# Kernel tuning notes

Measured on AMD Instinct MI355X. Metric: run time of the kernel, lower is better.

Reference implementation:

```python
import jax, jax.numpy as jnp
import numpy as np

N_NODES = 50000
N_EDGES = 1600000
IN_DIM, HID, HEADS, OUT_DIM = 128, 32, 4, 16
NEG_SLOPE = 0.2  # DGL GATConv default


def setup_inputs() -> dict:
    key = jax.random.key(0)
    ks = jax.random.split(key, 12)
    features = jax.random.normal(ks[0], (N_NODES, IN_DIM), dtype=jnp.float32)
    src = jax.random.randint(ks[1], (N_EDGES,), 0, N_NODES, dtype=jnp.int32)
    dst = jax.random.randint(ks[2], (N_EDGES,), 0, N_NODES, dtype=jnp.int32)
    # layer 1 params (xavier-style scale)
    W1 = jax.random.normal(ks[3], (IN_DIM, HEADS * HID), dtype=jnp.float32) * (2.0 / (IN_DIM + HEADS * HID)) ** 0.5
    al1 = jax.random.normal(ks[4], (HEADS, HID), dtype=jnp.float32) * 0.1
    ar1 = jax.random.normal(ks[5], (HEADS, HID), dtype=jnp.float32) * 0.1
    b1 = jnp.zeros((HEADS * HID,), dtype=jnp.float32)
    # layer 2 params
    W2 = jax.random.normal(ks[6], (HID, OUT_DIM), dtype=jnp.float32) * (2.0 / (HID + OUT_DIM)) ** 0.5
    al2 = jax.random.normal(ks[7], (1, OUT_DIM), dtype=jnp.float32) * 0.1
    ar2 = jax.random.normal(ks[8], (1, OUT_DIM), dtype=jnp.float32) * 0.1
    b2 = jnp.zeros((OUT_DIM,), dtype=jnp.float32)
    return {"features": features, "src": src, "dst": dst,
            "W1": W1, "al1": al1, "ar1": ar1, "b1": b1,
            "W2": W2, "al2": al2, "ar2": ar2, "b2": b2}


def gat_conv(x, src, dst, W, al, ar, b, n_nodes):
    """DGL GATConv (no dropout, no residual). Returns [N, H, out]."""
    H, out = al.shape
    feat = (x @ W).reshape(-1, H, out)                       # [N,H,out]
    el = jnp.sum(feat * al, axis=-1)                         # [N,H]
    er = jnp.sum(feat * ar, axis=-1)                         # [N,H]
    e = jax.nn.leaky_relu(el[src] + er[dst], NEG_SLOPE)      # [E,H]
    # segment softmax over incoming edges per destination node
    m = jax.ops.segment_max(e, dst, num_segments=n_nodes)    # [N,H]
    ex = jnp.exp(e - m[dst])                                 # [E,H]
    s = jax.ops.segment_sum(ex, dst, num_segments=n_nodes)   # [N,H]
    alpha = ex / s[dst]                                      # [E,H]
    msg = alpha[:, :, None] * feat[src]                      # [E,H,out]
    rst = jax.ops.segment_sum(msg, dst, num_segments=n_nodes)
    return rst + b.reshape(H, out)


def reference(features, src, dst, W1, al1, ar1, b1, W2, al2, ar2, b2):
    n = features.shape[0]
    x1 = gat_conv(features, src, dst, W1, al1, ar1, b1, n)   # [N,HEADS,HID]
    x1 = jnp.mean(jax.nn.relu(x1), axis=1)                   # [N,HID]
    x2 = gat_conv(x1, src, dst, W2, al2, ar2, b2, n)         # [N,1,OUT]
    x2 = jnp.squeeze(x2, axis=1)                             # [N,OUT]
    return jax.nn.log_softmax(x2, axis=-1)
```

## Files before the change

### kernel.cpp

```cpp
#include <hip/hip_runtime.h>
#include <math.h>

#define NEG_SLOPE 0.2f
#define BINCAP 10240

typedef __attribute__((ext_vector_type(8))) short short8;
typedef __attribute__((ext_vector_type(4))) float f32x4;
typedef __attribute__((ext_vector_type(2))) float f32x2;

__device__ __forceinline__ float lrelu(float x) {
    return x >= 0.f ? x : NEG_SLOPE * x;
}
__device__ __forceinline__ unsigned bf16_rne(float f) {
    unsigned b = __float_as_uint(f);
    return (b + 0x7FFFu + ((b >> 16) & 1u)) >> 16;
}

__global__ __launch_bounds__(256) void prep(
    const float* __restrict__ W, unsigned short* __restrict__ Wt,
    int* __restrict__ bin_cursor)
{
    if (blockIdx.x == 64) {
        bin_cursor[threadIdx.x] = threadIdx.x * BINCAP;
        return;
    }
    int i = blockIdx.x * 256 + threadIdx.x;
    int kin = i >> 7, nout = i & 127;
    Wt[nout * 128 + kin] = (unsigned short)bf16_rne(W[kin * 128 + nout]);
}

__global__ __launch_bounds__(256) void scatter_bins(
    const int* __restrict__ src, const int* __restrict__ dst,
    int* __restrict__ bin_cursor, unsigned* __restrict__ binned,
    int E, int nbins)
{
    __shared__ unsigned stage[3328];
    __shared__ int hist[256];
    __shared__ int base_l[256];
    int tid = threadIdx.x;
    hist[tid] = 0;
    __syncthreads();
    int epb = (E + gridDim.x - 1) / gridDim.x;
    int beg = blockIdx.x * epb, end = min(E, beg + epb);
    int cnt_local = end - beg;
    for (int k = tid; k < cnt_local; k += 256) {
        int d = dst[beg + k];
        stage[k] = ((unsigned)d << 16) | (unsigned)src[beg + k];
        atomicAdd(&hist[d >> 8], 1);
    }
    __syncthreads();
    if (tid < nbins) {
        int c = hist[tid];
        base_l[tid] = (c > 0) ? atomicAdd(&bin_cursor[tid], c) : 0;
    }
    __syncthreads();
    hist[tid] = 0;
    __syncthreads();
    for (int k = tid; k < cnt_local; k += 256) {
        unsigned w = stage[k];
        int bin = w >> 24;
        int slot = atomicAdd(&hist[bin], 1);
        binned[base_l[bin] + slot] = w;
    }
}

__global__ __launch_bounds__(256) void local_sort(
    const unsigned* __restrict__ binned, const int* __restrict__ bin_cursor,
    int* __restrict__ rowptr, unsigned short* __restrict__ deg,
    unsigned short* __restrict__ csr, int N, int nbins)
{
    __shared__ int cnt[256];
    __shared__ int sh[256];
    int b = blockIdx.x;
    int t = threadIdx.x;
    int gbase = b * BINCAP;
    int gcount = bin_cursor[b] - gbase;
    cnt[t] = 0;
    __syncthreads();
    for (int i = t; i < gcount; i += 256)
        atomicAdd(&cnt[(binned[gbase + i] >> 16) & 255], 1);
    __syncthreads();
    int own = cnt[t];
    sh[t] = own;
    __syncthreads();
#pragma unroll
    for (int off = 1; off < 256; off <<= 1) {
        int v = (t >= off) ? sh[t - off] : 0;
        __syncthreads();
        sh[t] += v;
        __syncthreads();
    }
    int excl = sh[t] - own;
    int dcount = min(256, N - (b << 8));
    if (t < dcount) {
        rowptr[(b << 8) + t] = gbase + excl;
        deg[(b << 8) + t] = (unsigned short)own;
    }
    cnt[t] = excl;
    __syncthreads();
    for (int i = t; i < gcount; i += 256) {
        unsigned w = binned[gbase + i];
        int slot = atomicAdd(&cnt[(w >> 16) & 255], 1);
        csr[gbase + slot] = (unsigned short)(w & 0xFFFFu);
    }
}

__global__ __launch_bounds__(256) void gemm1_mfma(
    const float* __restrict__ X, const unsigned short* __restrict__ Wt,
    const float* __restrict__ al, const float* __restrict__ ar,
    unsigned short* __restrict__ feat1b, float* __restrict__ el1,
    float* __restrict__ er1, int N)
{
    __shared__ unsigned short Xb[64][136];
    __shared__ unsigned short Wb[128][136];
    int tid = threadIdx.x;
    int nb = blockIdx.x * 64;

    for (int idx = tid; idx < 128 * 16; idx += 256) {
        int row = idx >> 4, q = idx & 15;
        *(uint4*)&Wb[row][q * 8] = *(const uint4*)&Wt[row * 128 + q * 8];
    }
    for (int idx = tid; idx < 64 * 32; idx += 256) {
        int row = idx >> 5, q = idx & 31;
        int n = nb + row;
        float4 v = (n < N) ? *(const float4*)&X[(size_t)n * 128 + q * 4]
                           : make_float4(0.f, 0.f, 0.f, 0.f);
        unsigned lo = bf16_rne(v.x) | (bf16_rne(v.y) << 16);
        unsigned hi = bf16_rne(v.z) | (bf16_rne(v.w) << 16);
        *(uint2*)&Xb[row][q * 4] = make_uint2(lo, hi);
    }
    __syncthreads();

    int wave = tid >> 6, lane = tid & 63;
    int m = lane & 15, quad = lane >> 4;
    f32x4 acc[8];
#pragma unroll
    for (int t = 0; t < 8; ++t) acc[t] = (f32x4){0.f, 0.f, 0.f, 0.f};

#pragma unroll
    for (int kt = 0; kt < 4; ++kt) {
        int k0 = kt * 32 + quad * 8;
        short8 a = *(const short8*)&Xb[wave * 16 + m][k0];
#pragma unroll
        for (int t = 0; t < 8; ++t) {
            short8 b = *(const short8*)&Wb[t * 16 + m][k0];
            acc[t] = __builtin_amdgcn_mfma_f32_16x16x32_bf16(a, b, acc[t], 0, 0, 0);
        }
    }

    float al_lo[4], al_hi[4], ar_lo[4], ar_hi[4];
#pragma unroll
    for (int h = 0; h < 4; ++h) {
        al_lo[h] = al[h * 32 + m];       al_hi[h] = al[h * 32 + 16 + m];
        ar_lo[h] = ar[h * 32 + m];       ar_hi[h] = ar[h * 32 + 16 + m];
    }

#pragma unroll
    for (int r = 0; r < 4; ++r) {
        int n = nb + wave * 16 + quad * 4 + r;
        float pel[4], per[4];
#pragma unroll
        for (int h = 0; h < 4; ++h) {
            float fa = acc[2 * h][r], fb = acc[2 * h + 1][r];
            pel[h] = fa * al_lo[h] + fb * al_hi[h];
            per[h] = fa * ar_lo[h] + fb * ar_hi[h];
        }
#pragma unroll
        for (int off = 1; off < 16; off <<= 1) {
#pragma unroll
            for (int h = 0; h < 4; ++h) {
                pel[h] += __shfl_xor(pel[h], off);
                per[h] += __shfl_xor(per[h], off);
            }
        }
        if (n < N) {
#pragma unroll
            for (int t = 0; t < 8; ++t)
                feat1b[(size_t)n * 128 + t * 16 + m] =
                    (unsigned short)bf16_rne(acc[t][r]);
            if (m == 0) {
#pragma unroll
                for (int h = 0; h < 4; ++h) {
                    el1[(size_t)n * 4 + h] = pel[h];
                    er1[(size_t)n * 4 + h] = per[h];
                }
            }
        }
    }
}

__global__ __launch_bounds__(256) void agg1_fused(
    const int* __restrict__ rowptr, const unsigned short* __restrict__ deg,
    const unsigned short* __restrict__ csr,
    const unsigned short* __restrict__ feat1b, const float* __restrict__ el1,
    const float* __restrict__ er1, const float* __restrict__ b1,
    const float* __restrict__ W2, const float* __restrict__ al2,
    const float* __restrict__ ar2, unsigned short* __restrict__ feat2b,
    float* __restrict__ el2, float* __restrict__ er2, int N)
{
    __shared__ uint2 pairs[4][4][66];
    int gid = blockIdx.x * 256 + threadIdx.x;
    int d = gid >> 6;
    if (d >= N) return;
    int wv = (threadIdx.x >> 6) & 3;
    int lane = threadIdx.x & 63;
    int h = lane >> 4;
    float4 er4 = ((const float4*)er1)[d];
    int beg = rowptr[d], end = beg + (int)deg[d];
    const unsigned* feat32 = (const unsigned*)feat1b;

    float M = -INFINITY, S = 0.f;
    f32x2 A = {0.f, 0.f};

    for (int base = beg; base < end; base += 64) {
        int cnt = min(64, end - base);
        int sn = 0;
        float4 v = make_float4(-INFINITY, -INFINITY, -INFINITY, -INFINITY);
        if (lane < cnt) {
            sn = (int)csr[base + lane];
            float4 el4 = ((const float4*)el1)[sn];
            v.x = lrelu(el4.x + er4.x);
            v.y = lrelu(el4.y + er4.y);
            v.z = lrelu(el4.z + er4.z);
            v.w = lrelu(el4.w + er4.w);
        }
        float4 cm = v;
#pragma unroll
        for (int off = 1; off < 64; off <<= 1) {
            cm.x = fmaxf(cm.x, __shfl_xor(cm.x, off));
            cm.y = fmaxf(cm.y, __shfl_xor(cm.y, off));
            cm.z = fmaxf(cm.z, __shfl_xor(cm.z, off));
            cm.w = fmaxf(cm.w, __shfl_xor(cm.w, off));
        }
        float4 w;
        w.x = __expf(v.x - cm.x);
        w.y = __expf(v.y - cm.y);
        w.z = __expf(v.z - cm.z);
        w.w = __expf(v.w - cm.w);
        unsigned snb = (unsigned)sn << 6;
        pairs[wv][0][lane] = make_uint2(snb, __float_as_uint(w.x));
        pairs[wv][1][lane] = make_uint2(snb, __float_as_uint(w.y));
        pairs[wv][2][lane] = make_uint2(snb, __float_as_uint(w.z));
        pairs[wv][3][lane] = make_uint2(snb, __float_as_uint(w.w));

        float cmh = (h & 2) ? ((h & 1) ? cm.w : cm.z) : ((h & 1) ? cm.y : cm.x);
        float nM = fmaxf(M, cmh);
        float so = __expf(M - nM);
        float sc = __expf(cmh - nM);
        M = nM;

        f32x2 ca = {0.f, 0.f};
        float cs = 0.f;
        for (int i = 0; i < cnt; ++i) {
            uint2 p = pairs[wv][h][i];
            float wb = __uint_as_float(p.y);
            unsigned u = feat32[p.x + lane];
            f32x2 f = {__uint_as_float(u << 16),
                       __uint_as_float(u & 0xFFFF0000u)};
            ca += (f32x2){wb, wb} * f;
            cs += wb;
        }
        S = S * so + cs * sc;
        A = A * (f32x2){so, so} + ca * (f32x2){sc, sc};
    }
    float inv = (end > beg) ? (1.f / S) : 0.f;
    float o0 = A.x * inv, o1 = A.y * inv;

    int dim0 = lane * 2;
    float2 bb = *(const float2*)(b1 + dim0);
    float r0 = fmaxf(o0 + bb.x, 0.f);
    float r1 = fmaxf(o1 + bb.y, 0.f);
    r0 += __shfl_xor(r0, 16); r0 += __shfl_xor(r0, 32);
    r1 += __shfl_xor(r1, 16); r1 += __shfl_xor(r1, 32);
    float u0 = 0.25f * r0;
    float u1 = 0.25f * r1;

    int j = lane & 15;
    float f2 = 0.f;
#pragma unroll
    for (int i = 0; i < 16; ++i) {
        float xa = __shfl(u0, i);
        float xb = __shfl(u1, i);
        f2 += xa * W2[(2 * i) * 16 + j] + xb * W2[(2 * i + 1) * 16 + j];
    }
    float pel = f2 * al2[j], per = f2 * ar2[j];
#pragma unroll
    for (int off = 1; off < 16; off <<= 1) {
        pel += __shfl_xor(pel, off);
        per += __shfl_xor(per, off);
    }
    if (lane < 16) feat2b[(size_t)d * 16 + j] = (unsigned short)bf16_rne(f2);
    if (lane == 0) { el2[d] = pel; er2[d] = per; }
}

__global__ __launch_bounds__(256) void agg2_fused(
    const int* __restrict__ rowptr, const unsigned short* __restrict__ deg,
    const unsigned short* __restrict__ csr,
    const unsigned short* __restrict__ feat2b, const float* __restrict__ el2,
    const float* __restrict__ er2, const float* __restrict__ b2,
    float* __restrict__ out, int N)
{
    __shared__ uint2 pairs2[4][64];
    int gid = blockIdx.x * 256 + threadIdx.x;
    int d = gid >> 6;
    if (d >= N) return;
    int wv = (threadIdx.x >> 6) & 3;
    int lane = threadIdx.x & 63;
    int sub = lane >> 4, dim = lane & 15;
    float er = er2[d];
    int beg = rowptr[d], end = beg + (int)deg[d];

    float M = -INFINITY, S = 0.f, a = 0.f;
    for (int cb = beg; cb < end; cb += 64) {
        int cnt = min(64, end - cb);
        int sn = 0;
        float v = -INFINITY;
        if (lane < cnt) {
            sn = (int)csr[cb + lane];
            v = lrelu(el2[sn] + er);
        }
        float cm = v;
#pragma unroll
        for (int off = 1; off < 64; off <<= 1)
            cm = fmaxf(cm, __shfl_xor(cm, off));
        float w = __expf(v - cm);
        float cs = w;
#pragma unroll
        for (int off = 1; off < 64; off <<= 1)
            cs += __shfl_xor(cs, off);
        pairs2[wv][lane] = make_uint2((unsigned)sn << 4, __float_as_uint(w));

        float nM = fmaxf(M, cm);
        float so = __expf(M - nM);
        float sc = __expf(cm - nM);
        M = nM;
        float ca = 0.f;
        for (int i = sub; i < cnt; i += 4) {
            uint2 p = pairs2[wv][i];
            float wb = __uint_as_float(p.y);
            unsigned u = (unsigned)feat2b[p.x + dim];
            ca += wb * __uint_as_float(u << 16);
        }
        S = S * so + cs * sc;
        a = a * so + ca * sc;
    }
    a += __shfl_xor(a, 16);
    a += __shfl_xor(a, 32);
    float inv = (end > beg) ? (1.f / S) : 0.f;
    float val = a * inv + b2[dim];
    float mm = val;
#pragma unroll
    for (int off = 1; off < 16; off <<= 1)
        mm = fmaxf(mm, __shfl_xor(mm, off));
    float ex = __expf(val - mm);
    float ssum = ex;
#pragma unroll
    for (int off = 1; off < 16; off <<= 1)
        ssum += __shfl_xor(ssum, off);
    if (lane < 16)
        out[(size_t)d * 16 + dim] = val - (mm + __logf(ssum));
}

extern "C" void kernel_launch(void* const* d_in, const int* in_sizes, int n_in,
                              void* d_out, int out_size, void* d_ws, size_t ws_size,
                              hipStream_t stream)
{
    const float* X   = (const float*)d_in[0];
    const int*   src = (const int*)d_in[1];
    const int*   dst = (const int*)d_in[2];
    const float* W1  = (const float*)d_in[3];
    const float* al1 = (const float*)d_in[4];
    const float* ar1 = (const float*)d_in[5];
    const float* b1  = (const float*)d_in[6];
    const float* W2  = (const float*)d_in[7];
    const float* al2 = (const float*)d_in[8];
    const float* ar2 = (const float*)d_in[9];
    const float* b2  = (const float*)d_in[10];
    int N = in_sizes[0] / 128;
    int E = in_sizes[1];
    int nbins = (N + 255) >> 8;

    float* ws = (float*)d_ws;
    size_t o = 0;
    unsigned short* feat1b = (unsigned short*)(ws + o); o += (size_t)N * 64;
    float* el1   = ws + o; o += (size_t)N * 4;
    float* er1   = ws + o; o += (size_t)N * 4;
    unsigned short* feat2b = (unsigned short*)(ws + o); o += (size_t)N * 8;
    float* el2   = ws + o; o += (size_t)N;
    float* er2   = ws + o; o += (size_t)N;
    int* rowptr  = (int*)(ws + o); o += (size_t)N;
    unsigned short* deg = (unsigned short*)(ws + o); o += (size_t)N / 2 + 1;
    unsigned short* Wt1b = (unsigned short*)(ws + o); o += 128 * 128 / 2;
    int* bin_cursor = (int*)(ws + o); o += 256;
    unsigned* binned = (unsigned*)(ws + o); o += (size_t)nbins * BINCAP;
    unsigned short* csr = (unsigned short*)(ws + o); o += (size_t)nbins * BINCAP / 2 + 1;
    float* out = (float*)d_out;

    prep<<<65, 256, 0, stream>>>(W1, Wt1b, bin_cursor);
    scatter_bins<<<512, 256, 0, stream>>>(src, dst, bin_cursor, binned, E, nbins);
    local_sort<<<nbins, 256, 0, stream>>>(binned, bin_cursor, rowptr, deg, csr, N, nbins);

    gemm1_mfma<<<(N + 63) / 64, 256, 0, stream>>>(X, Wt1b, al1, ar1, feat1b, el1, er1, N);

    agg1_fused<<<(N * 64 + 255) / 256, 256, 0, stream>>>(
        rowptr, deg, csr, feat1b, el1, er1, b1, W2, al2, ar2, feat2b, el2, er2, N);

    agg2_fused<<<(N * 64 + 255) / 256, 256, 0, stream>>>(
        rowptr, deg, csr, feat2b, el2, er2, b2, out, N);
}
```

Measured before the change: 251.0 us.

## Fuse GEMM1 and edge binning into one launch, unroll aggregation loops

Merges the prep, scatter_bins and gemm1 kernels into one heterogeneous launch. Some blocks run the bf16 MFMA GEMM, transposing and converting W1 in shared memory themselves, while the other blocks bin the edges. The bin cursor is zeroed with a memset and now holds relative counts. The aggregation inner loops in agg1 and agg2 are unrolled with two accumulators to raise memory-level parallelism. This removes launch overhead and lets the two independent phases overlap, but every GEMM block now redoes the W1 transpose and conversion, and the larger dynamic shared memory may lower occupancy.

```diff
diff --git a/kernel.cpp b/kernel.cpp
--- a/kernel.cpp
+++ b/kernel.cpp
@@ -16,51 +16,123 @@
     return (b + 0x7FFFu + ((b >> 16) & 1u)) >> 16;
 }
 
-__global__ __launch_bounds__(256) void prep(
-    const float* __restrict__ W, unsigned short* __restrict__ Wt,
-    int* __restrict__ bin_cursor)
-{
-    if (blockIdx.x == 64) {
-        bin_cursor[threadIdx.x] = threadIdx.x * BINCAP;
-        return;
-    }
-    int i = blockIdx.x * 256 + threadIdx.x;
-    int kin = i >> 7, nout = i & 127;
-    Wt[nout * 128 + kin] = (unsigned short)bf16_rne(W[kin * 128 + nout]);
-}
-
-__global__ __launch_bounds__(256) void scatter_bins(
+extern "C" __global__ __launch_bounds__(256) void gemm_scatter(
+    const float* __restrict__ X, const float* __restrict__ W1,
+    const float* __restrict__ al, const float* __restrict__ ar,
     const int* __restrict__ src, const int* __restrict__ dst,
     int* __restrict__ bin_cursor, unsigned* __restrict__ binned,
-    int E, int nbins)
+    unsigned short* __restrict__ feat1b, float* __restrict__ el1,
+    float* __restrict__ er1, int N, int E, int nbins, int gemm_blocks)
 {
-    __shared__ unsigned stage[3328];
-    __shared__ int hist[256];
-    __shared__ int base_l[256];
+    extern __shared__ char smem_raw[];
     int tid = threadIdx.x;
-    hist[tid] = 0;
+
+    if ((int)blockIdx.x >= gemm_blocks) {
+        unsigned* stage = (unsigned*)smem_raw;
+        int* hist   = (int*)(stage + 3328);
+        int* base_l = hist + 256;
+        int bid = blockIdx.x - gemm_blocks;
+        hist[tid] = 0;
+        __syncthreads();
+        int epb = (E + 511) / 512;
+        int beg = bid * epb, end = min(E, beg + epb);
+        int cnt_local = end - beg;
+        for (int k = tid; k < cnt_local; k += 256) {
+            int d = dst[beg + k];
+            stage[k] = ((unsigned)d << 16) | (unsigned)src[beg + k];
+            atomicAdd(&hist[d >> 8], 1);
+        }
+        __syncthreads();
+        if (tid < nbins) {
+            int c = hist[tid];
+            base_l[tid] = (c > 0) ? (tid * BINCAP + atomicAdd(&bin_cursor[tid], c)) : 0;
+        }
+        __syncthreads();
+        hist[tid] = 0;
+        __syncthreads();
+        for (int k = tid; k < cnt_local; k += 256) {
+            unsigned w = stage[k];
+            int bin = w >> 24;
+            int slot = atomicAdd(&hist[bin], 1);
+            binned[base_l[bin] + slot] = w;
+        }
+        return;
+    }
+
+    unsigned short* Xb = (unsigned short*)smem_raw;
+    unsigned short* Wb = Xb + 64 * 136;
+    int nb = blockIdx.x * 64;
+
+    for (int idx = tid; idx < 128 * 128; idx += 256) {
+        int kin = idx >> 7, nout = idx & 127;
+        Wb[nout * 138 + kin] = (unsigned short)bf16_rne(W1[idx]);
+    }
+    for (int idx = tid; idx < 64 * 32; idx += 256) {
+        int row = idx >> 5, q = idx & 31;
+        int n = nb + row;
+        float4 v = (n < N) ? *(const float4*)&X[(size_t)n * 128 + q * 4]
+                           : make_float4(0.f, 0.f, 0.f, 0.f);
+        unsigned lo = bf16_rne(v.x) | (bf16_rne(v.y) << 16);
+        unsigned hi = bf16_rne(v.z) | (bf16_rne(v.w) << 16);
+        *(uint2*)&Xb[row * 136 + q * 4] = make_uint2(lo, hi);
+    }
     __syncthreads();
-    int epb = (E + gridDim.x - 1) / gridDim.x;
-    int beg = blockIdx.x * epb, end = min(E, beg + epb);
-    int cnt_local = end - beg;
-    for (int k = tid; k < cnt_local; k += 256) {
-        int d = dst[beg + k];
-        stage[k] = ((unsigned)d << 16) | (unsigned)src[beg + k];
-        atomicAdd(&hist[d >> 8], 1);
-    }
-    __syncthreads();
-    if (tid < nbins) {
-        int c = hist[tid];
-        base_l[tid] = (c > 0) ? atomicAdd(&bin_cursor[tid], c) : 0;
-    }
-    __syncthreads();
-    hist[tid] = 0;
-    __syncthreads();
-    for (int k = tid; k < cnt_local; k += 256) {
-        unsigned w = stage[k];
-        int bin = w >> 24;
-        int slot = atomicAdd(&hist[bin], 1);
-        binned[base_l[bin] + slot] = w;
+
+    int wave = tid >> 6, lane = tid & 63;
+    int m = lane & 15, quad = lane >> 4;
+    f32x4 acc[8];
+#pragma unroll
+    for (int t = 0; t < 8; ++t) acc[t] = (f32x4){0.f, 0.f, 0.f, 0.f};
+
+#pragma unroll
+    for (int kt = 0; kt < 4; ++kt) {
+        int k0 = kt * 32 + quad * 8;
+        short8 a = *(const short8*)&Xb[(wave * 16 + m) * 136 + k0];
+#pragma unroll
+        for (int t = 0; t < 8; ++t) {
+            short8 b = *(const short8*)&Wb[(t * 16 + m) * 138 + k0];
+            acc[t] = __builtin_amdgcn_mfma_f32_16x16x32_bf16(a, b, acc[t], 0, 0, 0);
+        }
+    }
+
+    float al_lo[4], al_hi[4], ar_lo[4], ar_hi[4];
+#pragma unroll
+    for (int h = 0; h < 4; ++h) {
+        al_lo[h] = al[h * 32 + m];       al_hi[h] = al[h * 32 + 16 + m];
+        ar_lo[h] = ar[h * 32 + m];       ar_hi[h] = ar[h * 32 + 16 + m];
+    }
+
+#pragma unroll
+    for (int r = 0; r < 4; ++r) {
+        int n = nb + wave * 16 + quad * 4 + r;
+        float pel[4], per[4];
+#pragma unroll
+        for (int h = 0; h < 4; ++h) {
+            float fa = acc[2 * h][r], fb = acc[2 * h + 1][r];
+            pel[h] = fa * al_lo[h] + fb * al_hi[h];
+            per[h] = fa * ar_lo[h] + fb * ar_hi[h];
+        }
+#pragma unroll
+        for (int off = 1; off < 16; off <<= 1) {
+#pragma unroll
+            for (int h = 0; h < 4; ++h) {
+                pel[h] += __shfl_xor(pel[h], off);
+                per[h] += __shfl_xor(per[h], off);
+            }
+        }
+        if (n < N) {
+#pragma unroll
+            for (int t = 0; t < 8; ++t)
+                feat1b[(size_t)n * 128 + t * 16 + m] =
+                    (unsigned short)bf16_rne(acc[t][r]);
+            if (m == 0) {
+#pragma unroll
+                for (int h = 0; h < 4; ++h) {
+                    el1[(size_t)n * 4 + h] = pel[h];
+                    er1[(size_t)n * 4 + h] = per[h];
+                }
+            }
+        }
     }
 }
 
@@ -74,7 +146,7 @@
     int b = blockIdx.x;
     int t = threadIdx.x;
     int gbase = b * BINCAP;
-    int gcount = bin_cursor[b] - gbase;
+    int gcount = bin_cursor[b];
     cnt[t] = 0;
     __syncthreads();
     for (int i = t; i < gcount; i += 256)
@@ -102,90 +174,6 @@
         unsigned w = binned[gbase + i];
         int slot = atomicAdd(&cnt[(w >> 16) & 255], 1);
         csr[gbase + slot] = (unsigned short)(w & 0xFFFFu);
-    }
-}
-
-__global__ __launch_bounds__(256) void gemm1_mfma(
-    const float* __restrict__ X, const unsigned short* __restrict__ Wt,
-    const float* __restrict__ al, const float* __restrict__ ar,
-    unsigned short* __restrict__ feat1b, float* __restrict__ el1,
-    float* __restrict__ er1, int N)
-{
-    __shared__ unsigned short Xb[64][136];
-    __shared__ unsigned short Wb[128][136];
-    int tid = threadIdx.x;
-    int nb = blockIdx.x * 64;
-
-    for (int idx = tid; idx < 128 * 16; idx += 256) {
-        int row = idx >> 4, q = idx & 15;
-        *(uint4*)&Wb[row][q * 8] = *(const uint4*)&Wt[row * 128 + q * 8];
-    }
-    for (int idx = tid; idx < 64 * 32; idx += 256) {
-        int row = idx >> 5, q = idx & 31;
-        int n = nb + row;
-        float4 v = (n < N) ? *(const float4*)&X[(size_t)n * 128 + q * 4]
-                           : make_float4(0.f, 0.f, 0.f, 0.f);
-        unsigned lo = bf16_rne(v.x) | (bf16_rne(v.y) << 16);
-        unsigned hi = bf16_rne(v.z) | (bf16_rne(v.w) << 16);
-        *(uint2*)&Xb[row][q * 4] = make_uint2(lo, hi);
-    }
-    __syncthreads();
-
-    int wave = tid >> 6, lane = tid & 63;
-    int m = lane & 15, quad = lane >> 4;
-    f32x4 acc[8];
-#pragma unroll
-    for (int t = 0; t < 8; ++t) acc[t] = (f32x4){0.f, 0.f, 0.f, 0.f};
-
-#pragma unroll
-    for (int kt = 0; kt < 4; ++kt) {
-        int k0 = kt * 32 + quad * 8;
-        short8 a = *(const short8*)&Xb[wave * 16 + m][k0];
-#pragma unroll
-        for (int t = 0; t < 8; ++t) {
-            short8 b = *(const short8*)&Wb[t * 16 + m][k0];
-            acc[t] = __builtin_amdgcn_mfma_f32_16x16x32_bf16(a, b, acc[t], 0, 0, 0);
-        }
-    }
-
-    float al_lo[4], al_hi[4], ar_lo[4], ar_hi[4];
-#pragma unroll
-    for (int h = 0; h < 4; ++h) {
-        al_lo[h] = al[h * 32 + m];       al_hi[h] = al[h * 32 + 16 + m];
-        ar_lo[h] = ar[h * 32 + m];       ar_hi[h] = ar[h * 32 + 16 + m];
-    }
-
-#pragma unroll
-    for (int r = 0; r < 4; ++r) {
-        int n = nb + wave * 16 + quad * 4 + r;
-        float pel[4], per[4];
-#pragma unroll
-        for (int h = 0; h < 4; ++h) {
-            float fa = acc[2 * h][r], fb = acc[2 * h + 1][r];
-            pel[h] = fa * al_lo[h] + fb * al_hi[h];
-            per[h] = fa * ar_lo[h] + fb * ar_hi[h];
-        }
-#pragma unroll
-        for (int off = 1; off < 16; off <<= 1) {
-#pragma unroll
-            for (int h = 0; h < 4; ++h) {
-                pel[h] += __shfl_xor(pel[h], off);
-                per[h] += __shfl_xor(per[h], off);
-            }
-        }
-        if (n < N) {
-#pragma unroll
-            for (int t = 0; t < 8; ++t)
-                feat1b[(size_t)n * 128 + t * 16 + m] =
-                    (unsigned short)bf16_rne(acc[t][r]);
-            if (m == 0) {
-#pragma unroll
-                for (int h = 0; h < 4; ++h) {
-                    el1[(size_t)n * 4 + h] = pel[h];
-                    er1[(size_t)n * 4 + h] = per[h];
-                }
-            }
-        }
     }
 }
 
@@ -249,17 +237,41 @@
         float sc = __expf(cmh - nM);
         M = nM;
 
-        f32x2 ca = {0.f, 0.f};
-        float cs = 0.f;
-        for (int i = 0; i < cnt; ++i) {
+        f32x2 ca = {0.f, 0.f}, cb = {0.f, 0.f};
+        float cs0 = 0.f, cs1 = 0.f;
+        int i = 0;
+        for (; i + 4 <= cnt; i += 4) {
+            uint2 p0 = pairs[wv][h][i];
+            uint2 p1 = pairs[wv][h][i + 1];
+            uint2 p2 = pairs[wv][h][i + 2];
+            uint2 p3 = pairs[wv][h][i + 3];
+            unsigned u0 = feat32[p0.x + lane];
+            unsigned u1 = feat32[p1.x + lane];
+            unsigned u2 = feat32[p2.x + lane];
+            unsigned u3 = feat32[p3.x + lane];
+            float w0 = __uint_as_float(p0.y), w1 = __uint_as_float(p1.y);
+            float w2 = __uint_as_float(p2.y), w3 = __uint_as_float(p3.y);
+            ca += (f32x2){w0, w0} * (f32x2){__uint_as_float(u0 << 16),
+                                            __uint_as_float(u0 & 0xFFFF0000u)};
+            cb += (f32x2){w1, w1} * (f32x2){__uint_as_float(u1 << 16),
+                                            __uint_as_float(u1 & 0xFFFF0000u)};
+            ca += (f32x2){w2, w2} * (f32x2){__uint_as_float(u2 << 16),
+                                            __uint_as_float(u2 & 0xFFFF0000u)};
+            cb += (f32x2){w3, w3} * (f32x2){__uint_as_float(u3 << 16),
+                                            __uint_as_float(u3 & 0xFFFF0000u)};
+            cs0 += w0 + w2;
+            cs1 += w1 + w3;
+        }
+        for (; i < cnt; ++i) {
             uint2 p = pairs[wv][h][i];
             float wb = __uint_as_float(p.y);
             unsigned u = feat32[p.x + lane];
-            f32x2 f = {__uint_as_float(u << 16),
-                       __uint_as_float(u & 0xFFFF0000u)};
-            ca += (f32x2){wb, wb} * f;
-            cs += wb;
-        }
+            ca += (f32x2){wb, wb} * (f32x2){__uint_as_float(u << 16),
+                                            __uint_as_float(u & 0xFFFF0000u)};
+            cs0 += wb;
+        }
+        ca += cb;
+        float cs = cs0 + cs1;
         S = S * so + cs * sc;
         A = A * (f32x2){so, so} + ca * (f32x2){sc, sc};
     }
@@ -278,10 +290,10 @@
     int j = lane & 15;
     float f2 = 0.f;
 #pragma unroll
-    for (int i = 0; i < 16; ++i) {
-        float xa = __shfl(u0, i);
-        float xb = __shfl(u1, i);
-        f2 += xa * W2[(2 * i) * 16 + j] + xb * W2[(2 * i + 1) * 16 + j];
+    for (int i2 = 0; i2 < 16; ++i2) {
+        float xa = __shfl(u0, i2);
+        float xb = __shfl(u1, i2);
+        f2 += xa * W2[(2 * i2) * 16 + j] + xb * W2[(2 * i2 + 1) * 16 + j];
     }
     float pel = f2 * al2[j], per = f2 * ar2[j];
 #pragma unroll
@@ -334,15 +346,23 @@
         float so = __expf(M - nM);
         float sc = __expf(cm - nM);
         M = nM;
-        float ca = 0.f;
-        for (int i = sub; i < cnt; i += 4) {
+        float ca = 0.f, ca2 = 0.f;
+        int i = sub;
+        for (; i + 4 < cnt; i += 8) {
+            uint2 p0 = pairs2[wv][i];
+            uint2 p1 = pairs2[wv][i + 4];
+            unsigned u0 = (unsigned)feat2b[p0.x + dim];
+            unsigned u1 = (unsigned)feat2b[p1.x + dim];
+            ca  += __uint_as_float(p0.y) * __uint_as_float(u0 << 16);
+            ca2 += __uint_as_float(p1.y) * __uint_as_float(u1 << 16);
+        }
+        if (i < cnt) {
             uint2 p = pairs2[wv][i];
-            float wb = __uint_as_float(p.y);
             unsigned u = (unsigned)feat2b[p.x + dim];
-            ca += wb * __uint_as_float(u << 16);
+            ca += __uint_as_float(p.y) * __uint_as_float(u << 16);
         }
         S = S * so + cs * sc;
-        a = a * so + ca * sc;
+        a = a * so + (ca + ca2) * sc;
     }
     a += __shfl_xor(a, 16);
     a += __shfl_xor(a, 32);
@@ -390,17 +410,19 @@
     float* er2   = ws + o; o += (size_t)N;
     int* rowptr  = (int*)(ws + o); o += (size_t)N;
     unsigned short* deg = (unsigned short*)(ws + o); o += (size_t)N / 2 + 1;
-    unsigned short* Wt1b = (unsigned short*)(ws + o); o += 128 * 128 / 2;
     int* bin_cursor = (int*)(ws + o); o += 256;
     unsigned* binned = (unsigned*)(ws + o); o += (size_t)nbins * BINCAP;
     unsigned short* csr = (unsigned short*)(ws + o); o += (size_t)nbins * BINCAP / 2 + 1;
     float* out = (float*)d_out;
 
-    prep<<<65, 256, 0, stream>>>(W1, Wt1b, bin_cursor);
-    scatter_bins<<<512, 256, 0, stream>>>(src, dst, bin_cursor, binned, E, nbins);
+    hipMemsetAsync(bin_cursor, 0, 256 * sizeof(int), stream);
+
+    int gemm_blocks = (N + 63) / 64;
+    gemm_scatter<<<gemm_blocks + 512, 256, 52736, stream>>>(
+        X, W1, al1, ar1, src, dst, bin_cursor, binned,
+        feat1b, el1, er1, N, E, nbins, gemm_blocks);
+
     local_sort<<<nbins, 256, 0, stream>>>(binned, bin_cursor, rowptr, deg, csr, N, nbins);
-
-    gemm1_mfma<<<(N + 63) / 64, 256, 0, stream>>>(X, Wt1b, al1, ar1, feat1b, el1, er1, N);
 
     agg1_fused<<<(N * 64 + 255) / 256, 256, 0, stream>>>(
         rowptr, deg, csr, feat1b, el1, er1, b1, W2, al2, ar2, feat2b, el2, er2, N);
```

New measurement: 248.0 us. Within noise of the previous version (-1.2%).
